# Optimization experiments

Measured on AMD Instinct MI355X. Metric: run time of the kernel, lower is better.

The kernel has to match this reference:

```python
import jax, jax.numpy as jnp
import numpy as np

B, S, D = 2, 2048, 1024
H = 16
HD = D // H
SCALE = HD ** (-0.5)


def setup_inputs() -> dict:
    key = jax.random.key(0)
    k1, k2, k3, k4 = jax.random.split(key, 4)
    x = jax.random.normal(k1, (B, S, D), dtype=jnp.float32)
    # nn.Linear-style init scale to keep activations sane
    w_qkv = jax.random.normal(k2, (3 * D, D), dtype=jnp.float32) * (D ** -0.5)
    w_out = jax.random.normal(k3, (D, D), dtype=jnp.float32) * (D ** -0.5)
    b_out = jax.random.normal(k4, (D,), dtype=jnp.float32) * 0.01
    return {"x": x, "w_qkv": w_qkv, "w_out": w_out, "b_out": b_out}


def reference(x, w_qkv, w_out, b_out):
    b, s, d = x.shape
    # qkv projection (no bias): [b, s, 3d]
    qkv = jnp.einsum('bsd,ed->bse', x, w_qkv)
    # Rearrange 'b c (e h hd) -> e b h c hd'
    qkv = qkv.reshape(b, s, 3, H, HD).transpose(2, 0, 3, 1, 4)
    # NOTE: original splits as (v, q, k) in that order
    v, q, k = qkv[0], qkv[1], qkv[2]
    # scale applied after matmul, as in the original
    scores = jnp.einsum('bhqd,bhkd->bhqk', q, k) * SCALE
    attn = jax.nn.softmax(scores, axis=-1)
    o = jnp.einsum('bhqk,bhkd->bhqd', attn, v)
    # 'b h c hd -> b c (h hd)'
    o = o.transpose(0, 2, 1, 3).reshape(b, s, d)
    return jnp.einsum('bsd,ed->bse', o, w_out) + b_out
```

## Files before the change

kernel.cpp:

```cpp
#include <hip/hip_runtime.h>
#include <cstdint>
#include <cstddef>

#define BB 2
#define SS 2048
#define DD 1024
#define HH 16
#define HDIM 64

typedef short bf16x8 __attribute__((ext_vector_type(8)));
typedef short bf16x4 __attribute__((ext_vector_type(4)));
typedef float f32x4 __attribute__((ext_vector_type(4)));
typedef float f32x2 __attribute__((ext_vector_type(2)));

union U4S8 { uint4 u; bf16x8 s; };
union U2S4 { uint2 u; bf16x4 s; unsigned short h[4]; };

#if defined(__HIP_DEVICE_COMPILE__)
# if __has_builtin(__builtin_amdgcn_mfma_f32_16x16x16bf16_1k)
#  define MFMA_PV(a, b, c) __builtin_amdgcn_mfma_f32_16x16x16bf16_1k((a), (b), (c), 0, 0, 0)
# else
#  define MFMA_PV(a, b, c) __builtin_amdgcn_mfma_f32_16x16x16_bf16((a), (b), (c), 0, 0, 0)
# endif
# if __has_builtin(__builtin_amdgcn_exp2f)
#  define EXP2(x) __builtin_amdgcn_exp2f(x)
# else
#  define EXP2(x) exp2f(x)
# endif
#else
# define MFMA_PV(a, b, c) (c)
# define EXP2(x) exp2f(x)
#endif

__device__ __forceinline__ unsigned short f2bf(float f) {
    union { float f; unsigned int u; } c; c.f = f;
    unsigned int u = c.u;
    unsigned int r = (u + 0x7FFFu + ((u >> 16) & 1u)) >> 16;
    return (unsigned short)r;
}

__device__ __forceinline__ void async_cp16(const void* g, void* l) {
    __builtin_amdgcn_global_load_lds(
        (const __attribute__((address_space(1))) void*)g,
        (__attribute__((address_space(3))) void*)l, 16, 0, 0);
}

__global__ __launch_bounds__(256) void cvt_all(
    const float* __restrict__ x, const float* __restrict__ wq,
    const float* __restrict__ wo,
    unsigned short* __restrict__ xb, unsigned short* __restrict__ wqb,
    unsigned short* __restrict__ wob) {
    int i = blockIdx.x * 256 + threadIdx.x;
    const float* in; unsigned short* out; int j;
    if (i < 524288)       { in = x;  out = xb;  j = i; }
    else if (i < 917504)  { in = wq; out = wqb; j = i - 524288; }
    else                  { in = wo; out = wob; j = i - 917504; }
    float4 a = ((const float4*)in)[2 * j];
    float4 b = ((const float4*)in)[2 * j + 1];
    union { uint4 u; unsigned short h[8]; } o;
    o.h[0] = f2bf(a.x); o.h[1] = f2bf(a.y); o.h[2] = f2bf(a.z); o.h[3] = f2bf(a.w);
    o.h[4] = f2bf(b.x); o.h[5] = f2bf(b.y); o.h[6] = f2bf(b.z); o.h[7] = f2bf(b.w);
    ((uint4*)out)[j] = o.u;
}

__global__ __launch_bounds__(256) void gemm_qkv(
    const unsigned short* __restrict__ A,
    const unsigned short* __restrict__ Bw,
    unsigned short* __restrict__ qb, unsigned short* __restrict__ kb,
    unsigned short* __restrict__ vb) {
    const int K = 1024;
    __shared__ unsigned short smem[18432];
    int tid = threadIdx.x;
    int lane = tid & 63, wave = tid >> 6;
    int wm = (wave & 1) * 64, wn = (wave >> 1) * 64;
    int m0 = blockIdx.y * 128, n0 = blockIdx.x * 128;
    int lm = lane & 15, lq = lane >> 4;

    f32x4 acc[4][4] = {};

    int sdst = tid * 8;
    const unsigned short* gA = A  + (size_t)(m0 + (tid >> 2)) * K + (tid & 3) * 8;
    const unsigned short* gB = Bw + (size_t)(n0 + (tid >> 2)) * K + (tid & 3) * 8;

#define GSTAGE(k0, buf) do {                                          \
        async_cp16(gA + (k0),          smem + (buf) + sdst);          \
        async_cp16(gA + 64 * K + (k0), smem + (buf) + 2048 + sdst);   \
        async_cp16(gB + (k0),          smem + (buf) + 4096 + sdst);   \
        async_cp16(gB + 64 * K + (k0), smem + (buf) + 6144 + sdst);   \
    } while (0)

    GSTAGE(0, 0);
    for (int k0 = 0; k0 < K; k0 += 64) {
        #pragma unroll
        for (int hf = 0; hf < 2; hf++) {
            int base = hf ? 8192 : 0;
            int obuf = hf ? 0 : 8192;
            __syncthreads();
            int kn = k0 + 32 + hf * 32;
            if (kn < K) GSTAGE(kn, obuf);
            const unsigned short* As = smem + base;
            const unsigned short* Bs = smem + base + 4096;
            U4S8 af[4], bfx[4];
            #pragma unroll
            for (int i = 0; i < 4; i++) {
                af[i].u  = *(const uint4*)(As + (wm + i * 16 + lm) * 32 + lq * 8);
                bfx[i].u = *(const uint4*)(Bs + (wn + i * 16 + lm) * 32 + lq * 8);
            }
            #pragma unroll
            for (int mi = 0; mi < 4; mi++)
                #pragma unroll
                for (int ni = 0; ni < 4; ni++)
                    acc[mi][ni] = __builtin_amdgcn_mfma_f32_16x16x32_bf16(
                        af[mi].s, bfx[ni].s, acc[mi][ni], 0, 0, 0);
        }
    }
#undef GSTAGE
    __syncthreads();

    unsigned short* Lw = smem + wave * 4608;
    int b = m0 >> 11;
    int s_base = (m0 + wm) & 2047;
    if (n0 < 1024) {
        int h = (n0 + wn) >> 6;
        #pragma unroll
        for (int mi = 0; mi < 4; mi++)
            #pragma unroll
            for (int ni = 0; ni < 4; ni++)
                #pragma unroll
                for (int r = 0; r < 4; r++)
                    Lw[(ni * 16 + lm) * 72 + mi * 16 + lq * 4 + r] =
                        f2bf(acc[mi][ni][r]);
        __builtin_amdgcn_wave_barrier();
        unsigned short* vdst = vb + ((size_t)(b * HH + h) * HDIM) * SS + s_base;
        #pragma unroll
        for (int it = 0; it < 8; it++) {
            int hd = it * 8 + (lane >> 3);
            int so = (lane & 7) * 8;
            uint4 val = *(const uint4*)&Lw[hd * 72 + so];
            *(uint4*)(vdst + (size_t)hd * SS + so) = val;
        }
    } else {
        bool isq = n0 < 2048;
        unsigned short* dst = isq ? qb : kb;
        float scale = isq ? 0.18033688f : 1.0f;
        int h = ((n0 + wn) >> 6) & 15;
        #pragma unroll
        for (int mi = 0; mi < 4; mi++)
            #pragma unroll
            for (int ni = 0; ni < 4; ni++)
                #pragma unroll
                for (int r = 0; r < 4; r++)
                    Lw[(mi * 16 + lq * 4 + r) * 72 + ni * 16 + lm] =
                        f2bf(acc[mi][ni][r] * scale);
        __builtin_amdgcn_wave_barrier();
        unsigned short* qdst =
            dst + ((size_t)(b * HH + h) * SS + s_base) * HDIM;
        #pragma unroll
        for (int it = 0; it < 8; it++) {
            int srw = it * 8 + (lane >> 3);
            int so = (lane & 7) * 8;
            uint4 val = *(const uint4*)&Lw[srw * 72 + so];
            *(uint4*)(qdst + (size_t)srw * HDIM + so) = val;
        }
    }
}

__global__ __launch_bounds__(256) void attn(
    const unsigned short* __restrict__ qb,
    const unsigned short* __restrict__ kb,
    const unsigned short* __restrict__ vb,
    unsigned short* __restrict__ ob) {
    int bh = blockIdx.y;
    int q0 = blockIdx.x * 128;
    int tid = threadIdx.x, lane = tid & 63, wave = tid >> 6;
    int lm = lane & 15, lq = lane >> 4;

    __shared__ unsigned short smem[4 * 4096];

    const unsigned short* qg = qb + (size_t)bh * SS * HDIM;
    const unsigned short* kg = kb + (size_t)bh * SS * HDIM;
    const unsigned short* vg = vb + (size_t)bh * HDIM * SS;

    U4S8 qf[2][2];
    #pragma unroll
    for (int qt = 0; qt < 2; qt++)
        #pragma unroll
        for (int ks = 0; ks < 2; ks++)
            qf[qt][ks].u = *(const uint4*)(
                qg + (size_t)(q0 + wave * 32 + qt * 16 + lm) * HDIM + ks * 32 + lq * 8);

    f32x4 oacc[4][2] = {};
    f32x2 lsum2[2] = {};

    int lm7 = lm & 7;
    int kidx = lm * 64 + 8 * (lq ^ lm7);
    int vidx[4];
    #pragma unroll
    for (int kc = 0; kc < 4; kc++)
        vidx[kc] = lm * 64 + 8 * (((kc << 1) | (lq >> 1)) ^ lm7) + (lq & 1) * 4;

    int srow = tid >> 3;
    int scl  = (tid & 7) ^ (srow & 7);
    int sdst = tid * 8;
    const unsigned short* kptr = kg + (size_t)srow * HDIM + scl * 8;
    const unsigned short* vptr = vg + (size_t)srow * SS + scl * 8;

    #define STAGE(buf)                                                         \
        do {                                                                   \
            async_cp16(kptr,             smem + (buf) + sdst);                 \
            async_cp16(kptr + 32 * HDIM, smem + (buf) + 2048 + sdst);          \
            async_cp16(vptr,             smem + (buf) + 4096 + sdst);          \
            async_cp16(vptr + 32 * SS,   smem + (buf) + 6144 + sdst);          \
            kptr += 64 * HDIM; vptr += 64;                                     \
        } while (0)

    STAGE(0);

    for (int kt = 0; kt < SS / 64; kt += 2) {
        #pragma unroll
        for (int hf = 0; hf < 2; hf++) {
            int base = hf ? 8192 : 0;
            int obuf = hf ? 0 : 8192;
            __syncthreads();
            STAGE(obuf);

            U2S4 pb[4][2];
            #pragma unroll
            for (int mi = 0; mi < 4; mi++) {
                U4S8 kf0, kf1;
                kf0.u = *(const uint4*)(smem + base + mi * 1024 + kidx);
                kf1.u = *(const uint4*)(smem + base + mi * 1024 + (kidx ^ 32));
                #pragma unroll
                for (int qt = 0; qt < 2; qt++) {
                    f32x4 sa = {};
                    sa = __builtin_amdgcn_mfma_f32_16x16x32_bf16(kf0.s, qf[qt][0].s, sa, 0, 0, 0);
                    sa = __builtin_amdgcn_mfma_f32_16x16x32_bf16(kf1.s, qf[qt][1].s, sa, 0, 0, 0);
                    float p0 = EXP2(sa[0]);
                    float p1 = EXP2(sa[1]);
                    float p2 = EXP2(sa[2]);
                    float p3 = EXP2(sa[3]);
                    f32x2 a01; a01[0] = p0; a01[1] = p1;
                    f32x2 a23; a23[0] = p2; a23[1] = p3;
                    lsum2[qt] += a01;
                    lsum2[qt] += a23;
                    unsigned int b0 = __float_as_uint(p0) + 0x8000u;
                    unsigned int b1 = __float_as_uint(p1) + 0x8000u;
                    unsigned int b2 = __float_as_uint(p2) + 0x8000u;
                    unsigned int b3 = __float_as_uint(p3) + 0x8000u;
                    pb[mi][qt].u.x = __builtin_amdgcn_perm(b1, b0, 0x07060302u);
                    pb[mi][qt].u.y = __builtin_amdgcn_perm(b3, b2, 0x07060302u);
                }
            }

            #pragma unroll
            for (int mi2 = 0; mi2 < 4; mi2++) {
                #pragma unroll
                for (int kc = 0; kc < 4; kc++) {
                    U2S4 vf;
                    vf.u = *(const uint2*)(smem + base + 4096 + mi2 * 1024 + vidx[kc]);
                    oacc[mi2][0] = MFMA_PV(vf.s, pb[kc][0].s, oacc[mi2][0]);
                    oacc[mi2][1] = MFMA_PV(vf.s, pb[kc][1].s, oacc[mi2][1]);
                }
            }
        }
    }
    #undef STAGE

    float inv[2];
    #pragma unroll
    for (int qt = 0; qt < 2; qt++) {
        float s = lsum2[qt][0] + lsum2[qt][1];
        s += __shfl_xor(s, 16);
        s += __shfl_xor(s, 32);
        inv[qt] = 1.f / s;
    }

    __syncthreads();
    unsigned short* Ow = smem + wave * (32 * 72);
    #pragma unroll
    for (int mi2 = 0; mi2 < 4; mi2++)
        #pragma unroll
        for (int qt = 0; qt < 2; qt++) {
            U2S4 t;
            #pragma unroll
            for (int r = 0; r < 4; r++)
                t.h[r] = f2bf(oacc[mi2][qt][r] * inv[qt]);
            *(uint2*)&Ow[(qt * 16 + lm) * 72 + mi2 * 16 + lq * 4] = t.u;
        }
    __builtin_amdgcn_wave_barrier();
    int b = bh >> 4, h = bh & 15;
    #pragma unroll
    for (int it = 0; it < 4; it++) {
        int q  = it * 8 + (lane >> 3);
        int off = (lane & 7) * 8;
        uint4 val = *(const uint4*)&Ow[q * 72 + off];
        int srw = q0 + wave * 32 + q;
        *(uint4*)(ob + (size_t)(b * SS + srw) * DD + h * 64 + off) = val;
    }
}

__global__ __launch_bounds__(256) void gemm_out(
    const unsigned short* __restrict__ A,
    const unsigned short* __restrict__ Bw,
    const float* __restrict__ bias, float* __restrict__ out) {
    const int K = 1024;
    __shared__ unsigned short smem[12288];
    int tid = threadIdx.x;
    int lane = tid & 63, wave = tid >> 6;
    int wm = (wave & 1) * 64, wn = (wave >> 1) * 32;
    int m0 = blockIdx.y * 128, n0 = blockIdx.x * 64;
    int lm = lane & 15, lq = lane >> 4;

    f32x4 acc[4][2] = {};

    int sdst = tid * 8;
    const unsigned short* gA = A  + (size_t)(m0 + (tid >> 2)) * K + (tid & 3) * 8;
    const unsigned short* gB = Bw + (size_t)(n0 + (tid >> 2)) * K + (tid & 3) * 8;

#define OSTAGE(k0, buf) do {                                          \
        async_cp16(gA + (k0),          smem + (buf) + sdst);          \
        async_cp16(gA + 64 * K + (k0), smem + (buf) + 2048 + sdst);   \
        async_cp16(gB + (k0),          smem + (buf) + 4096 + sdst);   \
    } while (0)

    OSTAGE(0, 0);
    for (int k0 = 0; k0 < K; k0 += 64) {
        #pragma unroll
        for (int hf = 0; hf < 2; hf++) {
            int base = hf ? 6144 : 0;
            int obuf = hf ? 0 : 6144;
            __syncthreads();
            int kn = k0 + 32 + hf * 32;
            if (kn < K) OSTAGE(kn, obuf);
            const unsigned short* As = smem + base;
            const unsigned short* Bs = smem + base + 4096;
            U4S8 af[4], bfx[2];
            #pragma unroll
            for (int i = 0; i < 4; i++)
                af[i].u = *(const uint4*)(As + (wm + i * 16 + lm) * 32 + lq * 8);
            #pragma unroll
            for (int i = 0; i < 2; i++)
                bfx[i].u = *(const uint4*)(Bs + (wn + i * 16 + lm) * 32 + lq * 8);
            #pragma unroll
            for (int mi = 0; mi < 4; mi++)
                #pragma unroll
                for (int ni = 0; ni < 2; ni++)
                    acc[mi][ni] = __builtin_amdgcn_mfma_f32_16x16x32_bf16(
                        af[mi].s, bfx[ni].s, acc[mi][ni], 0, 0, 0);
        }
    }
#undef OSTAGE

    #pragma unroll
    for (int mi = 0; mi < 4; mi++) {
        int gr = m0 + wm + mi * 16 + lq * 4;
        #pragma unroll
        for (int ni = 0; ni < 2; ni++) {
            int gc = n0 + wn + ni * 16 + lm;
            float bv = bias[gc];
            #pragma unroll
            for (int r = 0; r < 4; r++)
                out[(size_t)(gr + r) * DD + gc] = acc[mi][ni][r] + bv;
        }
    }
}

extern "C" void kernel_launch(void* const* d_in, const int* in_sizes, int n_in,
                              void* d_out, int out_size, void* d_ws, size_t ws_size,
                              hipStream_t stream) {
    const float* x     = (const float*)d_in[0];
    const float* w_qkv = (const float*)d_in[1];
    const float* w_out = (const float*)d_in[2];
    const float* b_out = (const float*)d_in[3];
    float* out = (float*)d_out;

    unsigned short* ws = (unsigned short*)d_ws;
    const size_t NX = (size_t)BB * SS * DD;
    unsigned short* x_bf    = ws;
    unsigned short* wqkv_bf = x_bf + NX;
    unsigned short* wout_bf = wqkv_bf + 3145728;
    unsigned short* q_buf   = wout_bf + 1048576;
    unsigned short* k_buf   = q_buf + NX;
    unsigned short* v_buf   = k_buf + NX;
    unsigned short* o_buf   = v_buf + NX;

    cvt_all<<<4096, 256, 0, stream>>>(x, w_qkv, w_out, x_bf, wqkv_bf, wout_bf);
    gemm_qkv<<<dim3(24, 32), 256, 0, stream>>>(x_bf, wqkv_bf, q_buf, k_buf, v_buf);
    attn<<<dim3(16, 32), 256, 0, stream>>>(q_buf, k_buf, v_buf, o_buf);
    gemm_out<<<dim3(16, 32), 256, 0, stream>>>(o_buf, wout_bf, b_out, out);
}
```

Baseline: 205.0 us.

## Split attention KV sequence across two wave groups and merge partial outputs

```diff
diff --git a/kernel.cpp b/kernel.cpp
--- a/kernel.cpp
+++ b/kernel.cpp
@@ -165,7 +165,7 @@
     }
 }
 
-__global__ __launch_bounds__(256) void attn(
+__global__ __launch_bounds__(512) void attn(
     const unsigned short* __restrict__ qb,
     const unsigned short* __restrict__ kb,
     const unsigned short* __restrict__ vb,
@@ -173,9 +173,12 @@
     int bh = blockIdx.y;
     int q0 = blockIdx.x * 128;
     int tid = threadIdx.x, lane = tid & 63, wave = tid >> 6;
+    int grp = wave >> 2;
+    int w4  = wave & 3;
     int lm = lane & 15, lq = lane >> 4;
 
-    __shared__ unsigned short smem[4 * 4096];
+    __shared__ unsigned short smem[32768];
+    float* smf = (float*)smem;
 
     const unsigned short* qg = qb + (size_t)bh * SS * HDIM;
     const unsigned short* kg = kb + (size_t)bh * SS * HDIM;
@@ -187,7 +190,7 @@
         #pragma unroll
         for (int ks = 0; ks < 2; ks++)
             qf[qt][ks].u = *(const uint4*)(
-                qg + (size_t)(q0 + wave * 32 + qt * 16 + lm) * HDIM + ks * 32 + lq * 8);
+                qg + (size_t)(q0 + w4 * 32 + qt * 16 + lm) * HDIM + ks * 32 + lq * 8);
 
     f32x4 oacc[4][2] = {};
     f32x2 lsum2[2] = {};
@@ -200,36 +203,41 @@
         vidx[kc] = lm * 64 + 8 * (((kc << 1) | (lq >> 1)) ^ lm7) + (lq & 1) * 4;
 
     int srow = tid >> 3;
-    int scl  = (tid & 7) ^ (srow & 7);
+    int lch  = (tid & 7) ^ (srow & 7);
     int sdst = tid * 8;
-    const unsigned short* kptr = kg + (size_t)srow * HDIM + scl * 8;
-    const unsigned short* vptr = vg + (size_t)srow * SS + scl * 8;
-
-    #define STAGE(buf)                                                         \
+    const unsigned short* kpA = kg + (size_t)srow * HDIM + lch * 8;
+    const unsigned short* kpB = kpA + 64 * HDIM;
+    const unsigned short* vpA = vg + (size_t)srow * SS + lch * 8;
+    const unsigned short* vpB = vpA + 64;
+
+    #define STAGE(pbase)                                                       \
         do {                                                                   \
-            async_cp16(kptr,             smem + (buf) + sdst);                 \
-            async_cp16(kptr + 32 * HDIM, smem + (buf) + 2048 + sdst);          \
-            async_cp16(vptr,             smem + (buf) + 4096 + sdst);          \
-            async_cp16(vptr + 32 * SS,   smem + (buf) + 6144 + sdst);          \
-            kptr += 64 * HDIM; vptr += 64;                                     \
+            async_cp16(kpA, smem + (pbase) + sdst);                            \
+            async_cp16(kpB, smem + (pbase) + 4096 + sdst);                     \
+            async_cp16(vpA, smem + (pbase) + 8192 + sdst);                     \
+            async_cp16(vpB, smem + (pbase) + 12288 + sdst);                    \
+            kpA += 128 * HDIM; kpB += 128 * HDIM; vpA += 128; vpB += 128;      \
         } while (0)
 
     STAGE(0);
 
-    for (int kt = 0; kt < SS / 64; kt += 2) {
+    for (int kt = 0; kt < SS / 128; kt += 2) {
         #pragma unroll
         for (int hf = 0; hf < 2; hf++) {
-            int base = hf ? 8192 : 0;
-            int obuf = hf ? 0 : 8192;
+            int cbase = hf ? 16384 : 0;
+            int obase = hf ? 0 : 16384;
             __syncthreads();
-            STAGE(obuf);
+            STAGE(obase);
+
+            int kbase = cbase + grp * 4096;
+            int vbase = cbase + 8192 + grp * 4096;
 
             U2S4 pb[4][2];
             #pragma unroll
             for (int mi = 0; mi < 4; mi++) {
                 U4S8 kf0, kf1;
-                kf0.u = *(const uint4*)(smem + base + mi * 1024 + kidx);
-                kf1.u = *(const uint4*)(smem + base + mi * 1024 + (kidx ^ 32));
+                kf0.u = *(const uint4*)(smem + kbase + mi * 1024 + kidx);
+                kf1.u = *(const uint4*)(smem + kbase + mi * 1024 + (kidx ^ 32));
                 #pragma unroll
                 for (int qt = 0; qt < 2; qt++) {
                     f32x4 sa = {};
@@ -257,7 +265,7 @@
                 #pragma unroll
                 for (int kc = 0; kc < 4; kc++) {
                     U2S4 vf;
-                    vf.u = *(const uint2*)(smem + base + 4096 + mi2 * 1024 + vidx[kc]);
+                    vf.u = *(const uint2*)(smem + vbase + mi2 * 1024 + vidx[kc]);
                     oacc[mi2][0] = MFMA_PV(vf.s, pb[kc][0].s, oacc[mi2][0]);
                     oacc[mi2][1] = MFMA_PV(vf.s, pb[kc][1].s, oacc[mi2][1]);
                 }
@@ -266,36 +274,67 @@
     }
     #undef STAGE
 
-    float inv[2];
+    float gsum[2];
     #pragma unroll
     for (int qt = 0; qt < 2; qt++) {
         float s = lsum2[qt][0] + lsum2[qt][1];
         s += __shfl_xor(s, 16);
         s += __shfl_xor(s, 32);
-        inv[qt] = 1.f / s;
+        gsum[qt] = s;
     }
 
     __syncthreads();
-    unsigned short* Ow = smem + wave * (32 * 72);
-    #pragma unroll
-    for (int mi2 = 0; mi2 < 4; mi2++)
-        #pragma unroll
-        for (int qt = 0; qt < 2; qt++) {
-            U2S4 t;
-            #pragma unroll
-            for (int r = 0; r < 4; r++)
-                t.h[r] = f2bf(oacc[mi2][qt][r] * inv[qt]);
-            *(uint2*)&Ow[(qt * 16 + lm) * 72 + mi2 * 16 + lq * 4] = t.u;
-        }
-    __builtin_amdgcn_wave_barrier();
-    int b = bh >> 4, h = bh & 15;
-    #pragma unroll
-    for (int it = 0; it < 4; it++) {
-        int q  = it * 8 + (lane >> 3);
-        int off = (lane & 7) * 8;
-        uint4 val = *(const uint4*)&Ow[q * 72 + off];
-        int srw = q0 + wave * 32 + q;
-        *(uint4*)(ob + (size_t)(b * SS + srw) * DD + h * 64 + off) = val;
+
+    if (grp == 1) {
+        float* pub = smf + w4 * 2048;
+        #pragma unroll
+        for (int mi2 = 0; mi2 < 4; mi2++)
+            #pragma unroll
+            for (int qt = 0; qt < 2; qt++)
+                #pragma unroll
+                for (int r = 0; r < 4; r++)
+                    pub[(mi2 * 8 + qt * 4 + r) * 64 + lane] = oacc[mi2][qt][r];
+        if (lq == 0) {
+            smf[8192 + w4 * 32 + lm]      = gsum[0];
+            smf[8192 + w4 * 32 + 16 + lm] = gsum[1];
+        }
+    }
+    __syncthreads();
+
+    if (grp == 0) {
+        float* pub = smf + w4 * 2048;
+        #pragma unroll
+        for (int mi2 = 0; mi2 < 4; mi2++)
+            #pragma unroll
+            for (int qt = 0; qt < 2; qt++)
+                #pragma unroll
+                for (int r = 0; r < 4; r++)
+                    oacc[mi2][qt][r] += pub[(mi2 * 8 + qt * 4 + r) * 64 + lane];
+        float inv[2];
+        inv[0] = 1.f / (gsum[0] + smf[8192 + w4 * 32 + lm]);
+        inv[1] = 1.f / (gsum[1] + smf[8192 + w4 * 32 + 16 + lm]);
+
+        unsigned short* Ow = smem + 17024 + w4 * 2304;
+        #pragma unroll
+        for (int mi2 = 0; mi2 < 4; mi2++)
+            #pragma unroll
+            for (int qt = 0; qt < 2; qt++) {
+                U2S4 t;
+                #pragma unroll
+                for (int r = 0; r < 4; r++)
+                    t.h[r] = f2bf(oacc[mi2][qt][r] * inv[qt]);
+                *(uint2*)&Ow[(qt * 16 + lm) * 72 + mi2 * 16 + lq * 4] = t.u;
+            }
+        __builtin_amdgcn_wave_barrier();
+        int b = bh >> 4, h = bh & 15;
+        #pragma unroll
+        for (int it = 0; it < 4; it++) {
+            int q  = it * 8 + (lane >> 3);
+            int off = (lane & 7) * 8;
+            uint4 val = *(const uint4*)&Ow[q * 72 + off];
+            int srw = q0 + w4 * 32 + q;
+            *(uint4*)(ob + (size_t)(b * SS + srw) * DD + h * 64 + off) = val;
+        }
     }
 }
 
@@ -386,6 +425,6 @@
 
     cvt_all<<<4096, 256, 0, stream>>>(x, w_qkv, w_out, x_bf, wqkv_bf, wout_bf);
     gemm_qkv<<<dim3(24, 32), 256, 0, stream>>>(x_bf, wqkv_bf, q_buf, k_buf, v_buf);
-    attn<<<dim3(16, 32), 256, 0, stream>>>(q_buf, k_buf, v_buf, o_buf);
+    attn<<<dim3(16, 32), 512, 0, stream>>>(q_buf, k_buf, v_buf, o_buf);
     gemm_out<<<dim3(16, 32), 256, 0, stream>>>(o_buf, wout_bf, b_out, out);
 }
```

Result: faster. 200.7 us (-2.1%).
